# Performance work log

Hardware: AMD Instinct MI355X
Metric: run time of the kernel (lower is better)

The kernel has to match this reference:

```python
import jax, jax.numpy as jnp
import numpy as np

NEG_SLOPE = 0.2  # PyG GATConv default


def gat_conv(x, src, dst, W_src, W_dst, a_src, a_dst, b):
    """PyG GATConv with concat=False (mean over heads) and bias.
    x: [N, F_in]; src/dst: [E]; W_*: [F_in, H*D]; a_*: [H, D]; b: [D]."""
    N = x.shape[0]
    H, D = a_src.shape
    hs = (x @ W_src).reshape(N, H, D)
    hd = (x @ W_dst).reshape(N, H, D)
    al_s = (hs * a_src).sum(-1)  # [N, H]
    al_d = (hd * a_dst).sum(-1)  # [N, H]
    logits = jax.nn.leaky_relu(al_s[src] + al_d[dst], NEG_SLOPE)  # [E, H]
    # segment softmax over incoming edges of each dst node
    m = jax.lax.stop_gradient(jax.ops.segment_max(logits, dst, num_segments=N))
    e = jnp.exp(logits - m[dst])
    denom = jax.ops.segment_sum(e, dst, num_segments=N)  # [N, H]
    alpha = e / denom[dst]  # [E, H]
    msg = alpha[:, :, None] * hs[src]  # [E, H, D]
    out = jax.ops.segment_sum(msg, dst, num_segments=N)  # [N, H, D]
    return out.mean(axis=1) + b  # concat=False -> mean over heads


def setup_inputs() -> dict:
    key = jax.random.key(0)
    ks = jax.random.split(key, 12)
    N, F, Dh, H, E = 100000, 128, 128, 1, 1600000
    s = 0.05
    return {
        "x": jax.random.normal(ks[0], (N, F), jnp.float32),
        "edge_index": jax.random.randint(ks[1], (2, E), 0, N, jnp.int32),
        "W1_src": jax.random.normal(ks[2], (F, H * Dh), jnp.float32) * s,
        "W1_dst": jax.random.normal(ks[3], (F, H * Dh), jnp.float32) * s,
        "a1_src": jax.random.normal(ks[4], (H, Dh), jnp.float32) * s,
        "a1_dst": jax.random.normal(ks[5], (H, Dh), jnp.float32) * s,
        "b1": jnp.zeros((Dh,), jnp.float32),
        "W2_src": jax.random.normal(ks[6], (Dh, H * Dh), jnp.float32) * s,
        "W2_dst": jax.random.normal(ks[7], (Dh, H * Dh), jnp.float32) * s,
        "a2_src": jax.random.normal(ks[8], (H, Dh), jnp.float32) * s,
        "a2_dst": jax.random.normal(ks[9], (H, Dh), jnp.float32) * s,
        "b2": jnp.zeros((Dh,), jnp.float32),
    }


def reference(x, edge_index, W1_src, W1_dst, a1_src, a1_dst, b1,
              W2_src, W2_dst, a2_src, a2_dst, b2):
    src, dst = edge_index[0], edge_index[1]
    h = gat_conv(x, src, dst, W1_src, W1_dst, a1_src, a1_dst, b1)
    h = jax.nn.relu(h)  # ReLU between layers, none after the last
    out = gat_conv(h, src, dst, W2_src, W2_dst, a2_src, a2_dst, b2)
    return out
```

## Files before the change

kernel.cpp:

```cpp
#include <hip/hip_runtime.h>
#include <hip/hip_bf16.h>
#include <hip/hip_fp16.h>
#include <math.h>
#include <type_traits>


#define BKT_SHIFT 8
#define MAX_NB 512
#define EPB 2048

typedef _Float16 half8 __attribute__((ext_vector_type(8)));
typedef float floatx4 __attribute__((ext_vector_type(4)));

__global__ void convert_w_kernel(const float* __restrict__ W1,
                                 const float* __restrict__ W2,
                                 __half* __restrict__ wt1,
                                 __half* __restrict__ wt2) {
    const float* W = (blockIdx.x >> 4) ? W2 : W1;
    __half* WT = (blockIdx.x >> 4) ? wt2 : wt1;
    const int sub = blockIdx.x & 15;
    const int k0 = (sub >> 2) * 32, c0 = (sub & 3) * 32;
    __shared__ float t[32][33];
    const int r = threadIdx.x >> 5, c = threadIdx.x & 31;
    for (int rr = r; rr < 32; rr += 8)
        t[rr][c] = W[(size_t)(k0 + rr) * 128 + c0 + c];
    __syncthreads();
    for (int rr = r; rr < 32; rr += 8)
        WT[(size_t)(c0 + rr) * 128 + k0 + c] = __float2half_rn(t[c][rr]);
}

__global__ void make_wv4_kernel(const float* __restrict__ W1s,
                                const float* __restrict__ a1s,
                                const float* __restrict__ W1d,
                                const float* __restrict__ a1d,
                                const float* __restrict__ W2s,
                                const float* __restrict__ a2s,
                                const float* __restrict__ W2d,
                                const float* __restrict__ a2d,
                                float* __restrict__ wv) {
    const float* Wt[4] = {W1s, W1d, W2s, W2d};
    const float* at[4] = {a1s, a1d, a2s, a2d};
    const float* W = Wt[blockIdx.x];
    const float* a = at[blockIdx.x];
    int k = threadIdx.x;
    float s = 0.f;
    for (int d = 0; d < 128; ++d) s += W[k * 128 + d] * a[d];
    wv[blockIdx.x * 128 + k] = s;
}

template <typename InT>
__global__ void compute_al_kernel(const InT* __restrict__ X,
                                  const float* __restrict__ wsv,
                                  const float* __restrict__ wdv,
                                  float* __restrict__ al_s,
                                  float* __restrict__ al_d, int N) {
    int node = (int)((blockIdx.x * (unsigned)blockDim.x + threadIdx.x) >> 6);
    int lane = threadIdx.x & 63;
    if (node >= N) return;
    float2 xv;
    if constexpr (std::is_same<InT, float>::value) {
        xv = *(const float2*)&X[(size_t)node * 128 + lane * 2];
    } else {
        xv = __half22float2(*(const __half2*)&X[(size_t)node * 128 + lane * 2]);
    }
    float2 sv = *(const float2*)&wsv[lane * 2];
    float2 dv = *(const float2*)&wdv[lane * 2];
    float ps = xv.x * sv.x + xv.y * sv.y;
    float pd = xv.x * dv.x + xv.y * dv.y;
    for (int o = 32; o >= 1; o >>= 1) {
        ps += __shfl_xor(ps, o);
        pd += __shfl_xor(pd, o);
    }
    if (lane == 0) { al_s[node] = ps; al_d[node] = pd; }
}

__global__ void bucket_count_kernel(const int* __restrict__ dst,
                                    int* __restrict__ counts, int E, int NB) {
    __shared__ int h[MAX_NB];
    for (int i = threadIdx.x; i < NB; i += 256) h[i] = 0;
    __syncthreads();
    const int base = blockIdx.x * EPB;
#pragma unroll
    for (int j = 0; j < EPB / 256; ++j) {
        int i = base + j * 256 + threadIdx.x;
        if (i < E) atomicAdd(&h[dst[i] >> BKT_SHIFT], 1);
    }
    __syncthreads();
    for (int i = threadIdx.x; i < NB; i += 256)
        counts[(size_t)blockIdx.x * NB + i] = h[i];
}

__global__ void bucket_prefix_kernel(int* __restrict__ counts,
                                     int* __restrict__ totals, int NBLK,
                                     int NB) {
    __shared__ int lsum[256];
    const int b = blockIdx.x;
    const int t = threadIdx.x;
    int v[4];
    const int base = t * 4;
#pragma unroll
    for (int k = 0; k < 4; ++k) {
        int blk = base + k;
        v[k] = (blk < NBLK) ? counts[(size_t)blk * NB + b] : 0;
    }
    int s = v[0] + v[1] + v[2] + v[3];
    lsum[t] = s;
    __syncthreads();
    for (int o = 1; o < 256; o <<= 1) {
        int u = (t >= o) ? lsum[t - o] : 0;
        __syncthreads();
        lsum[t] += u;
        __syncthreads();
    }
    int run = lsum[t] - s;
#pragma unroll
    for (int k = 0; k < 4; ++k) {
        int blk = base + k;
        if (blk < NBLK) counts[(size_t)blk * NB + b] = run;
        run += v[k];
    }
    if (t == 255) totals[b] = lsum[255];
}

__global__ void bucket_base_kernel(const int* __restrict__ totals,
                                   int* __restrict__ bbase, int NB) {
    __shared__ int sh[MAX_NB];
    int t = threadIdx.x;
    int v = (t < NB) ? totals[t] : 0;
    sh[t] = v;
    __syncthreads();
    for (int o = 1; o < MAX_NB; o <<= 1) {
        int u = (t >= o) ? sh[t - o] : 0;
        __syncthreads();
        sh[t] += u;
        __syncthreads();
    }
    if (t < NB) bbase[t] = sh[t] - v;
}

__global__ void bucket_place_kernel(const int* __restrict__ src,
                                    const int* __restrict__ dst,
                                    const int* __restrict__ prefix,
                                    const int* __restrict__ bbase,
                                    int* __restrict__ bsrc,
                                    int* __restrict__ bdst, int E, int NB) {
    __shared__ int cur[MAX_NB];
    const int blk = blockIdx.x;
    for (int i = threadIdx.x; i < NB; i += 256)
        cur[i] = bbase[i] + prefix[(size_t)blk * NB + i];
    __syncthreads();
    const int base = blk * EPB;
#pragma unroll
    for (int j = 0; j < EPB / 256; ++j) {
        int i = base + j * 256 + threadIdx.x;
        if (i < E) {
            int d = dst[i], s = src[i];
            int p = atomicAdd(&cur[d >> BKT_SHIFT], 1);
            bsrc[p] = s;
            bdst[p] = d;
        }
    }
}

__global__ void bucket_csr_kernel(const int* __restrict__ bsrc,
                                  const int* __restrict__ bdst,
                                  const int* __restrict__ bbase,
                                  int* __restrict__ row_ptr,
                                  int* __restrict__ col, int N, int E,
                                  int NB) {
    __shared__ int cnt[256];
    __shared__ int cur[256];
    const int b = blockIdx.x;
    const int t = threadIdx.x;
    const int node0 = b << BKT_SHIFT;
    const int s = bbase[b];
    const int e = (b + 1 < NB) ? bbase[b + 1] : E;
    cnt[t] = 0;
    __syncthreads();
    for (int i = s + t; i < e; i += 256) atomicAdd(&cnt[bdst[i] & 255], 1);
    __syncthreads();
    int v = cnt[t];
    cur[t] = v;
    __syncthreads();
    for (int o = 1; o < 256; o <<= 1) {
        int u = (t >= o) ? cur[t - o] : 0;
        __syncthreads();
        cur[t] += u;
        __syncthreads();
    }
    int start = cur[t] - v;
    if (node0 + t < N) row_ptr[node0 + t] = s + start;
    __syncthreads();
    cur[t] = s + start;
    __syncthreads();
    for (int i = s + t; i < e; i += 256) {
        int d = bdst[i] & 255, sr = bsrc[i];
        int p = atomicAdd(&cur[d], 1);
        col[p] = sr;
    }
    if (b == 0 && t == 0) row_ptr[N] = E;
}

template <typename InT>
__global__ __launch_bounds__(256) void gemm_mfma_kernel(
    const InT* __restrict__ X, const __half* __restrict__ WT,
    __half* __restrict__ C, int N) {
    __shared__ __align__(16) __half Ws[128][136];
    __shared__ __align__(16) __half Xs[64][136];
    const int tid = threadIdx.x;
    const int row0 = blockIdx.x * 64;

    {
        int cr = tid >> 1, off = (tid & 1) * 64;
        const __half* srcp = &WT[(size_t)cr * 128 + off];
#pragma unroll
        for (int q = 0; q < 8; ++q)
            *(float4*)&Ws[cr][off + q * 8] = *(const float4*)&srcp[q * 8];
    }
    {
        int xr = tid >> 2, co = (tid & 3) * 32;
        int gr = row0 + xr;
        if constexpr (std::is_same<InT, float>::value) {
#pragma unroll
            for (int q = 0; q < 4; ++q) {
                float4 lo = make_float4(0.f, 0.f, 0.f, 0.f);
                float4 hi = make_float4(0.f, 0.f, 0.f, 0.f);
                if (gr < N) {
                    lo = *(const float4*)&X[(size_t)gr * 128 + co + q * 8];
                    hi = *(const float4*)&X[(size_t)gr * 128 + co + q * 8 + 4];
                }
                __align__(16) __half2 tmp[4];
                tmp[0] = __floats2half2_rn(lo.x, lo.y);
                tmp[1] = __floats2half2_rn(lo.z, lo.w);
                tmp[2] = __floats2half2_rn(hi.x, hi.y);
                tmp[3] = __floats2half2_rn(hi.z, hi.w);
                *(float4*)&Xs[xr][co + q * 8] = *(const float4*)tmp;
            }
        } else {
#pragma unroll
            for (int q = 0; q < 4; ++q) {
                float4 vz = make_float4(0.f, 0.f, 0.f, 0.f);
                if (gr < N)
                    vz = *(const float4*)&X[(size_t)gr * 128 + co + q * 8];
                *(float4*)&Xs[xr][co + q * 8] = vz;
            }
        }
    }
    __syncthreads();

    const int wid = tid >> 6;
    const int lane = tid & 63;
    const int lr = lane & 15, ks = lane >> 4;
    floatx4 acc[8];
#pragma unroll
    for (int t = 0; t < 8; ++t) acc[t] = (floatx4){0.f, 0.f, 0.f, 0.f};

#pragma unroll
    for (int kk = 0; kk < 4; ++kk) {
        half8 a = *(const half8*)&Xs[wid * 16 + lr][kk * 32 + ks * 8];
#pragma unroll
        for (int t = 0; t < 8; ++t) {
            half8 b = *(const half8*)&Ws[t * 16 + lr][kk * 32 + ks * 8];
            acc[t] = __builtin_amdgcn_mfma_f32_16x16x32_f16(a, b, acc[t], 0, 0, 0);
        }
    }
#pragma unroll
    for (int r = 0; r < 4; ++r) {
        int grow = row0 + wid * 16 + ks * 4 + r;
        if (grow < N) {
#pragma unroll
            for (int t = 0; t < 8; ++t)
                C[(size_t)grow * 128 + t * 16 + lr] = __float2half_rn(acc[t][r]);
        }
    }
}

template <typename OutT, bool RELU>
__global__ __launch_bounds__(256) void gat_aggregate_fused(
    const __half* __restrict__ hs, const float* __restrict__ al_s,
    const float* __restrict__ al_d, const int* __restrict__ row_ptr,
    const int* __restrict__ col, const float* __restrict__ bias,
    OutT* __restrict__ out, int N) {
    __shared__ int2 pairs[4][64];
    const int wid = threadIdx.x >> 6;
    int node = (int)((blockIdx.x * 256u + threadIdx.x) >> 6);
    int lane = threadIdx.x & 63;
    if (node >= N) return;
    const int begin = row_ptr[node], end = row_ptr[node + 1];
    const float ald = al_d[node];
    const int dblk = (lane & 15) * 8;
    const int slot = lane >> 4;

    float acc[8] = {0.f, 0.f, 0.f, 0.f, 0.f, 0.f, 0.f, 0.f};
    float den = 0.f;

    for (int base = begin; base < end; base += 64) {
        const int cnt = min(64, end - base);
        int idx = 0;
        float w = 0.f;
        if (lane < cnt) {
            idx = col[base + lane];
            float l = al_s[idx] + ald;
            l = (l >= 0.f) ? l : 0.2f * l;
            w = __expf(l);
        }
        float ws = w;
#pragma unroll
        for (int o = 32; o >= 1; o >>= 1) ws += __shfl_xor(ws, o);
        den += ws;
        pairs[wid][lane] = make_int2(idx, __float_as_int(w));

        const int ng = (cnt + 3) >> 2;
        int g = 0;
        for (; g + 4 <= ng; g += 4) {
            int2 pr[4];
            float4 raw[4];
#pragma unroll
            for (int u = 0; u < 4; ++u) pr[u] = pairs[wid][(g + u) * 4 + slot];
#pragma unroll
            for (int u = 0; u < 4; ++u)
                raw[u] = *(const float4*)&hs[((unsigned)pr[u].x << 7) + dblk];
#pragma unroll
            for (int u = 0; u < 4; ++u) {
                float wu = __int_as_float(pr[u].y);
                const __half2* hp = (const __half2*)&raw[u];
#pragma unroll
                for (int q = 0; q < 4; ++q) {
                    float2 f = __half22float2(hp[q]);
                    acc[2 * q]     = fmaf(wu, f.x, acc[2 * q]);
                    acc[2 * q + 1] = fmaf(wu, f.y, acc[2 * q + 1]);
                }
            }
        }
        for (; g < ng; ++g) {
            int2 pr = pairs[wid][g * 4 + slot];
            float4 raw = *(const float4*)&hs[((unsigned)pr.x << 7) + dblk];
            float wu = __int_as_float(pr.y);
            const __half2* hp = (const __half2*)&raw;
#pragma unroll
            for (int q = 0; q < 4; ++q) {
                float2 f = __half22float2(hp[q]);
                acc[2 * q]     = fmaf(wu, f.x, acc[2 * q]);
                acc[2 * q + 1] = fmaf(wu, f.y, acc[2 * q + 1]);
            }
        }
    }
#pragma unroll
    for (int r = 0; r < 8; ++r) {
        acc[r] += __shfl_xor(acc[r], 16);
        acc[r] += __shfl_xor(acc[r], 32);
    }
    if (slot == 0) {
        const float rden = (den > 0.f) ? 1.f / den : 0.f;
        float4 b0 = *(const float4*)&bias[dblk];
        float4 b1 = *(const float4*)&bias[dblk + 4];
        float o[8];
        o[0] = acc[0] * rden + b0.x; o[1] = acc[1] * rden + b0.y;
        o[2] = acc[2] * rden + b0.z; o[3] = acc[3] * rden + b0.w;
        o[4] = acc[4] * rden + b1.x; o[5] = acc[5] * rden + b1.y;
        o[6] = acc[6] * rden + b1.z; o[7] = acc[7] * rden + b1.w;
        if (RELU) {
#pragma unroll
            for (int r = 0; r < 8; ++r) o[r] = fmaxf(o[r], 0.f);
        }
        if constexpr (std::is_same<OutT, __half>::value) {
            __align__(16) __half2 hh[4];
#pragma unroll
            for (int q = 0; q < 4; ++q)
                hh[q] = __floats2half2_rn(o[2 * q], o[2 * q + 1]);
            *(float4*)&out[(size_t)node * 128 + dblk] = *(const float4*)hh;
        } else {
            *(float4*)&out[(size_t)node * 128 + dblk] =
                make_float4(o[0], o[1], o[2], o[3]);
            *(float4*)&out[(size_t)node * 128 + dblk + 4] =
                make_float4(o[4], o[5], o[6], o[7]);
        }
    }
}

extern "C" void kernel_launch(void* const* d_in, const int* in_sizes, int n_in,
                              void* d_out, int out_size, void* d_ws,
                              size_t ws_size, hipStream_t stream) {
    const float* x    = (const float*)d_in[0];
    const int*  eidx  = (const int*)d_in[1];
    const float* W1s  = (const float*)d_in[2];
    const float* W1d  = (const float*)d_in[3];
    const float* a1s  = (const float*)d_in[4];
    const float* a1d  = (const float*)d_in[5];
    const float* b1   = (const float*)d_in[6];
    const float* W2s  = (const float*)d_in[7];
    const float* W2d  = (const float*)d_in[8];
    const float* a2s  = (const float*)d_in[9];
    const float* a2d  = (const float*)d_in[10];
    const float* b2   = (const float*)d_in[11];

    const int N = in_sizes[0] / 128;
    const int E = in_sizes[1] / 2;
    const int* src = eidx;
    const int* dst = eidx + E;

    const int NB   = (N + 255) >> BKT_SHIFT;
    const int NBLK = (E + EPB - 1) / EPB;

    char* p = (char*)d_ws;
    auto alloc = [&](size_t bytes) {
        char* r = p;
        p += (bytes + 255) & ~(size_t)255;
        return r;
    };
    __half* hsA   = (__half*)alloc((size_t)N * 128 * 2);
    __half* h1    = (__half*)alloc((size_t)N * 128 * 2);
    int*   row_ptr= (int*)alloc((size_t)(N + 1) * 4);
    int*   col    = (int*)alloc((size_t)E * 4);
    int*   bsrc   = (int*)alloc((size_t)E * 4);
    int*   bdst   = (int*)alloc((size_t)E * 4);
    int*   counts = (int*)alloc((size_t)NBLK * NB * 4);
    int*   totals = (int*)alloc(MAX_NB * 4);
    int*   bbase  = (int*)alloc(MAX_NB * 4);
    float* al_s   = (float*)alloc((size_t)N * 4);
    float* al_d   = (float*)alloc((size_t)N * 4);
    float* wv     = (float*)alloc(4 * 128 * 4);
    __half* wt1   = (__half*)alloc(128 * 128 * 2);
    __half* wt2   = (__half*)alloc(128 * 128 * 2);

    convert_w_kernel<<<32, 256, 0, stream>>>(W1s, W2s, wt1, wt2);
    make_wv4_kernel<<<4, 128, 0, stream>>>(W1s, a1s, W1d, a1d, W2s, a2s, W2d,
                                           a2d, wv);

    bucket_count_kernel<<<NBLK, 256, 0, stream>>>(dst, counts, E, NB);
    bucket_prefix_kernel<<<NB, 256, 0, stream>>>(counts, totals, NBLK, NB);
    bucket_base_kernel<<<1, MAX_NB, 0, stream>>>(totals, bbase, NB);
    bucket_place_kernel<<<NBLK, 256, 0, stream>>>(src, dst, counts, bbase,
                                                  bsrc, bdst, E, NB);
    bucket_csr_kernel<<<NB, 256, 0, stream>>>(bsrc, bdst, bbase, row_ptr, col,
                                              N, E, NB);

    const int gemm_grid = (N + 63) / 64;
    const int wave_grid = (N + 3) / 4;

    gemm_mfma_kernel<float><<<gemm_grid, 256, 0, stream>>>(x, wt1, hsA, N);
    compute_al_kernel<float><<<wave_grid, 256, 0, stream>>>(
        x, wv + 0, wv + 128, al_s, al_d, N);
    gat_aggregate_fused<__half, true><<<wave_grid, 256, 0, stream>>>(
        hsA, al_s, al_d, row_ptr, col, b1, h1, N);

    gemm_mfma_kernel<__half><<<gemm_grid, 256, 0, stream>>>(h1, wt2, hsA, N);
    compute_al_kernel<__half><<<wave_grid, 256, 0, stream>>>(
        h1, wv + 256, wv + 384, al_s, al_d, N);
    gat_aggregate_fused<float, false><<<wave_grid, 256, 0, stream>>>(
        hsA, al_s, al_d, row_ptr, col, b2, (float*)d_out, N);
}
```

Before: 289.4 us.

## Pack bucket src/dst into one word and restructure aggregation to per-lane feature pairs

Bucket placement now writes a single packed int holding the low destination bits and the source id, replacing the two separate src and dst arrays and halving that intermediate traffic. The aggregation kernel drops the LDS pair buffer and 4-slot split. Each lane now owns two features and the wave walks edges 8 at a time, broadcasting indices and weights by shuffle, which removes the final cross-slot reduction. Packing assumes node ids fit in 17 bits. The new gather does narrower per-lane loads, issues redundant loads in padded tail iterations, and processes one edge per wave at a time.

Result: faster. 262.2 us (-9.4%).

```diff
diff --git a/kernel.cpp b/kernel.cpp
--- a/kernel.cpp
+++ b/kernel.cpp
@@ -142,8 +142,7 @@
                                     const int* __restrict__ dst,
                                     const int* __restrict__ prefix,
                                     const int* __restrict__ bbase,
-                                    int* __restrict__ bsrc,
-                                    int* __restrict__ bdst, int E, int NB) {
+                                    int* __restrict__ bpack, int E, int NB) {
     __shared__ int cur[MAX_NB];
     const int blk = blockIdx.x;
     for (int i = threadIdx.x; i < NB; i += 256)
@@ -156,14 +155,12 @@
         if (i < E) {
             int d = dst[i], s = src[i];
             int p = atomicAdd(&cur[d >> BKT_SHIFT], 1);
-            bsrc[p] = s;
-            bdst[p] = d;
-        }
-    }
-}
-
-__global__ void bucket_csr_kernel(const int* __restrict__ bsrc,
-                                  const int* __restrict__ bdst,
+            bpack[p] = ((d & 255) << 17) | s;
+        }
+    }
+}
+
+__global__ void bucket_csr_kernel(const int* __restrict__ bpack,
                                   const int* __restrict__ bbase,
                                   int* __restrict__ row_ptr,
                                   int* __restrict__ col, int N, int E,
@@ -177,7 +174,7 @@
     const int e = (b + 1 < NB) ? bbase[b + 1] : E;
     cnt[t] = 0;
     __syncthreads();
-    for (int i = s + t; i < e; i += 256) atomicAdd(&cnt[bdst[i] & 255], 1);
+    for (int i = s + t; i < e; i += 256) atomicAdd(&cnt[bpack[i] >> 17], 1);
     __syncthreads();
     int v = cnt[t];
     cur[t] = v;
@@ -194,9 +191,9 @@
     cur[t] = s + start;
     __syncthreads();
     for (int i = s + t; i < e; i += 256) {
-        int d = bdst[i] & 255, sr = bsrc[i];
-        int p = atomicAdd(&cur[d], 1);
-        col[p] = sr;
+        int pk = bpack[i];
+        int p = atomicAdd(&cur[pk >> 17], 1);
+        col[p] = pk & 0x1FFFF;
     }
     if (b == 0 && t == 0) row_ptr[N] = E;
 }
@@ -281,26 +278,21 @@
     const float* __restrict__ al_d, const int* __restrict__ row_ptr,
     const int* __restrict__ col, const float* __restrict__ bias,
     OutT* __restrict__ out, int N) {
-    __shared__ int2 pairs[4][64];
-    const int wid = threadIdx.x >> 6;
     int node = (int)((blockIdx.x * 256u + threadIdx.x) >> 6);
     int lane = threadIdx.x & 63;
     if (node >= N) return;
     const int begin = row_ptr[node], end = row_ptr[node + 1];
     const float ald = al_d[node];
-    const int dblk = (lane & 15) * 8;
-    const int slot = lane >> 4;
-
-    float acc[8] = {0.f, 0.f, 0.f, 0.f, 0.f, 0.f, 0.f, 0.f};
-    float den = 0.f;
-
+    const int d0 = lane * 2;
+
+    float acc0 = 0.f, acc1 = 0.f, den = 0.f;
     for (int base = begin; base < end; base += 64) {
         const int cnt = min(64, end - base);
-        int idx = 0;
+        int myidx = 0;
         float w = 0.f;
         if (lane < cnt) {
-            idx = col[base + lane];
-            float l = al_s[idx] + ald;
+            myidx = col[base + lane];
+            float l = al_s[myidx] + ald;
             l = (l >= 0.f) ? l : 0.2f * l;
             w = __expf(l);
         }
@@ -308,73 +300,32 @@
 #pragma unroll
         for (int o = 32; o >= 1; o >>= 1) ws += __shfl_xor(ws, o);
         den += ws;
-        pairs[wid][lane] = make_int2(idx, __float_as_int(w));
-
-        const int ng = (cnt + 3) >> 2;
-        int g = 0;
-        for (; g + 4 <= ng; g += 4) {
-            int2 pr[4];
-            float4 raw[4];
-#pragma unroll
-            for (int u = 0; u < 4; ++u) pr[u] = pairs[wid][(g + u) * 4 + slot];
-#pragma unroll
-            for (int u = 0; u < 4; ++u)
-                raw[u] = *(const float4*)&hs[((unsigned)pr[u].x << 7) + dblk];
-#pragma unroll
-            for (int u = 0; u < 4; ++u) {
-                float wu = __int_as_float(pr[u].y);
-                const __half2* hp = (const __half2*)&raw[u];
-#pragma unroll
-                for (int q = 0; q < 4; ++q) {
-                    float2 f = __half22float2(hp[q]);
-                    acc[2 * q]     = fmaf(wu, f.x, acc[2 * q]);
-                    acc[2 * q + 1] = fmaf(wu, f.y, acc[2 * q + 1]);
-                }
+
+        for (int e = 0; e < cnt; e += 8) {
+            __half2 v[8];
+            float we[8];
+#pragma unroll
+            for (int j = 0; j < 8; ++j) {
+                int s = __shfl(myidx, e + j);
+                we[j] = __shfl(w, e + j);
+                v[j] = *(const __half2*)&hs[((size_t)(unsigned)s << 7) + d0];
             }
-        }
-        for (; g < ng; ++g) {
-            int2 pr = pairs[wid][g * 4 + slot];
-            float4 raw = *(const float4*)&hs[((unsigned)pr.x << 7) + dblk];
-            float wu = __int_as_float(pr.y);
-            const __half2* hp = (const __half2*)&raw;
-#pragma unroll
-            for (int q = 0; q < 4; ++q) {
-                float2 f = __half22float2(hp[q]);
-                acc[2 * q]     = fmaf(wu, f.x, acc[2 * q]);
-                acc[2 * q + 1] = fmaf(wu, f.y, acc[2 * q + 1]);
+#pragma unroll
+            for (int j = 0; j < 8; ++j) {
+                float2 f = __half22float2(v[j]);
+                acc0 = fmaf(we[j], f.x, acc0);
+                acc1 = fmaf(we[j], f.y, acc1);
             }
         }
     }
-#pragma unroll
-    for (int r = 0; r < 8; ++r) {
-        acc[r] += __shfl_xor(acc[r], 16);
-        acc[r] += __shfl_xor(acc[r], 32);
-    }
-    if (slot == 0) {
-        const float rden = (den > 0.f) ? 1.f / den : 0.f;
-        float4 b0 = *(const float4*)&bias[dblk];
-        float4 b1 = *(const float4*)&bias[dblk + 4];
-        float o[8];
-        o[0] = acc[0] * rden + b0.x; o[1] = acc[1] * rden + b0.y;
-        o[2] = acc[2] * rden + b0.z; o[3] = acc[3] * rden + b0.w;
-        o[4] = acc[4] * rden + b1.x; o[5] = acc[5] * rden + b1.y;
-        o[6] = acc[6] * rden + b1.z; o[7] = acc[7] * rden + b1.w;
-        if (RELU) {
-#pragma unroll
-            for (int r = 0; r < 8; ++r) o[r] = fmaxf(o[r], 0.f);
-        }
-        if constexpr (std::is_same<OutT, __half>::value) {
-            __align__(16) __half2 hh[4];
-#pragma unroll
-            for (int q = 0; q < 4; ++q)
-                hh[q] = __floats2half2_rn(o[2 * q], o[2 * q + 1]);
-            *(float4*)&out[(size_t)node * 128 + dblk] = *(const float4*)hh;
-        } else {
-            *(float4*)&out[(size_t)node * 128 + dblk] =
-                make_float4(o[0], o[1], o[2], o[3]);
-            *(float4*)&out[(size_t)node * 128 + dblk + 4] =
-                make_float4(o[4], o[5], o[6], o[7]);
-        }
+    const float rden = (den > 0.f) ? 1.f / den : 0.f;
+    float o0 = acc0 * rden + bias[d0];
+    float o1 = acc1 * rden + bias[d0 + 1];
+    if (RELU) { o0 = fmaxf(o0, 0.f); o1 = fmaxf(o1, 0.f); }
+    if constexpr (std::is_same<OutT, __half>::value) {
+        *(__half2*)&out[(size_t)node * 128 + d0] = __floats2half2_rn(o0, o1);
+    } else {
+        *(float2*)&out[(size_t)node * 128 + d0] = make_float2(o0, o1);
     }
 }
 
@@ -412,8 +363,7 @@
     __half* h1    = (__half*)alloc((size_t)N * 128 * 2);
     int*   row_ptr= (int*)alloc((size_t)(N + 1) * 4);
     int*   col    = (int*)alloc((size_t)E * 4);
-    int*   bsrc   = (int*)alloc((size_t)E * 4);
-    int*   bdst   = (int*)alloc((size_t)E * 4);
+    int*   bpack  = (int*)alloc((size_t)E * 4);
     int*   counts = (int*)alloc((size_t)NBLK * NB * 4);
     int*   totals = (int*)alloc(MAX_NB * 4);
     int*   bbase  = (int*)alloc(MAX_NB * 4);
@@ -431,9 +381,9 @@
     bucket_prefix_kernel<<<NB, 256, 0, stream>>>(counts, totals, NBLK, NB);
     bucket_base_kernel<<<1, MAX_NB, 0, stream>>>(totals, bbase, NB);
     bucket_place_kernel<<<NBLK, 256, 0, stream>>>(src, dst, counts, bbase,
-                                                  bsrc, bdst, E, NB);
-    bucket_csr_kernel<<<NB, 256, 0, stream>>>(bsrc, bdst, bbase, row_ptr, col,
-                                              N, E, NB);
+                                                  bpack, E, NB);
+    bucket_csr_kernel<<<NB, 256, 0, stream>>>(bpack, bbase, row_ptr, col, N, E,
+                                              NB);
 
     const int gemm_grid = (N + 63) / 64;
     const int wave_grid = (N + 3) / 4;
```
